# Kernel optimization log

Measured on AMD Instinct MI355X. Metric: run time of the kernel, lower is better.

## Reference

```python
import jax, jax.numpy as jnp
import numpy as np


def setup_inputs() -> dict:
    key = jax.random.key(0)
    k1, k2, k3 = jax.random.split(key, 3)
    B, S, H = 64, 2048, 1024
    return {
        "dec_state_h": jax.random.normal(k1, (B, H), dtype=jnp.float32),
        "dec_state_c": jax.random.normal(k2, (B, H), dtype=jnp.float32),
        "enc_output": jax.random.normal(k3, (B, S, H), dtype=jnp.float32),
    }


def reference(dec_state_h, dec_state_c, enc_output):
    # dec_state: [B, H] = h + c  (Luong-style combined decoder state)
    dec_state = dec_state_h + dec_state_c
    # score[b, s] = sum_h enc_output[b, s, h] * dec_state[b, h]  -> [B, S, 1]
    score = jnp.einsum("bsh,bh->bs", enc_output, dec_state)[..., None]
    # softmax over the sequence axis
    attention_weights = jax.nn.softmax(score, axis=1)  # [B, S, 1]
    # context[b, h] = sum_s attn[b, s] * enc_output[b, s, h]
    context_vector = jnp.einsum("bs,bsh->bh", attention_weights[..., 0], enc_output)
    return context_vector, attention_weights
```

## Files before the change

### kernel.cpp

```cpp
#include <hip/hip_runtime.h>
#include <math.h>

#define B 64
#define S 2048
#define H 1024
#define SPLIT 16
#define ROWS_PER_BLOCK (S / SPLIT)
#define THREADS 256
#define WAVES 4
#define ROWS_PER_WAVE (ROWS_PER_BLOCK / WAVES)

__global__ __launch_bounds__(THREADS)
void luong_pass1(const float* __restrict__ dec_h,
                 const float* __restrict__ dec_c,
                 const float* __restrict__ enc,
                 float* __restrict__ attn_raw,
                 float* __restrict__ ctx_part,
                 float* __restrict__ mz_part) {
  const int bid  = blockIdx.x;
  const int b    = bid / SPLIT;
  const int sp   = bid % SPLIT;
  const int t    = threadIdx.x;
  const int w    = t >> 6;
  const int lane = t & 63;

  float4 dec[4];
  const float4* dh = (const float4*)(dec_h + (size_t)b * H);
  const float4* dc = (const float4*)(dec_c + (size_t)b * H);
#pragma unroll
  for (int c = 0; c < 4; ++c) {
    float4 a  = dh[c * 64 + lane];
    float4 bb = dc[c * 64 + lane];
    dec[c] = make_float4(a.x + bb.x, a.y + bb.y, a.z + bb.z, a.w + bb.w);
  }

  float m = -INFINITY;
  float Z = 0.f;
  float ctx[16];
#pragma unroll
  for (int k = 0; k < 16; ++k) ctx[k] = 0.f;

  const int s_base = sp * ROWS_PER_BLOCK + w;
  for (int r = 0; r < ROWS_PER_WAVE; ++r) {
    const int s = s_base + r * WAVES;
    const float4* erow = (const float4*)(enc + ((size_t)b * S + s) * H);
    float4 e[4];
#pragma unroll
    for (int c = 0; c < 4; ++c) e[c] = erow[c * 64 + lane];

    float partial = 0.f;
#pragma unroll
    for (int c = 0; c < 4; ++c)
      partial += e[c].x * dec[c].x + e[c].y * dec[c].y +
                 e[c].z * dec[c].z + e[c].w * dec[c].w;
#pragma unroll
    for (int off = 32; off >= 1; off >>= 1)
      partial += __shfl_xor(partial, off, 64);
    const float score = partial;

    if (lane == 0) attn_raw[b * S + s] = score;

    if (score > m) {
      const float f = expf(m - score);
      Z *= f;
#pragma unroll
      for (int k = 0; k < 16; ++k) ctx[k] *= f;
      m = score;
    }
    const float p = expf(score - m);
    Z += p;
#pragma unroll
    for (int c = 0; c < 4; ++c) {
      ctx[c * 4 + 0] += p * e[c].x;
      ctx[c * 4 + 1] += p * e[c].y;
      ctx[c * 4 + 2] += p * e[c].z;
      ctx[c * 4 + 3] += p * e[c].w;
    }
  }

  __shared__ float ctx_lds[WAVES][H];
  __shared__ float mzs[WAVES][2];
#pragma unroll
  for (int c = 0; c < 4; ++c) {
    float4 v = make_float4(ctx[c * 4 + 0], ctx[c * 4 + 1],
                           ctx[c * 4 + 2], ctx[c * 4 + 3]);
    ((float4*)&ctx_lds[w][c * 256])[lane] = v;
  }
  if (lane == 0) { mzs[w][0] = m; mzs[w][1] = Z; }
  __syncthreads();

  const float M = fmaxf(fmaxf(mzs[0][0], mzs[1][0]),
                        fmaxf(mzs[2][0], mzs[3][0]));
  float fac[WAVES];
  float Zb = 0.f;
#pragma unroll
  for (int i = 0; i < WAVES; ++i) {
    fac[i] = expf(mzs[i][0] - M);
    Zb += mzs[i][1] * fac[i];
  }

  float* outp = ctx_part + ((size_t)b * SPLIT + sp) * H;
#pragma unroll
  for (int q = 0; q < 4; ++q) {
    const int h = q * 256 + t;
    float v = 0.f;
#pragma unroll
    for (int i = 0; i < WAVES; ++i) v += ctx_lds[i][h] * fac[i];
    outp[h] = v;
  }
  if (t == 0) {
    mz_part[(b * SPLIT + sp) * 2 + 0] = M;
    mz_part[(b * SPLIT + sp) * 2 + 1] = Zb;
  }
}

__global__ __launch_bounds__(256)
void luong_combine(const float* __restrict__ ctx_part,
                   const float* __restrict__ mz_part,
                   float* __restrict__ ctx_out,
                   float* __restrict__ mz_final) {
  const int b = blockIdx.x;
  const int t = threadIdx.x;

  float m_i[SPLIT], z_i[SPLIT];
  float M = -INFINITY;
#pragma unroll
  for (int i = 0; i < SPLIT; ++i) {
    m_i[i] = mz_part[(b * SPLIT + i) * 2 + 0];
    z_i[i] = mz_part[(b * SPLIT + i) * 2 + 1];
    M = fmaxf(M, m_i[i]);
  }
  float fac[SPLIT];
  float Z = 0.f;
#pragma unroll
  for (int i = 0; i < SPLIT; ++i) {
    fac[i] = expf(m_i[i] - M);
    Z += z_i[i] * fac[i];
  }
  const float invZ = 1.f / Z;

#pragma unroll
  for (int q = 0; q < 4; ++q) {
    const int h = q * 256 + t;
    float v = 0.f;
#pragma unroll
    for (int i = 0; i < SPLIT; ++i)
      v += ctx_part[((size_t)(b * SPLIT + i)) * H + h] * fac[i];
    ctx_out[(size_t)b * H + h] = v * invZ;
  }
  if (t == 0) {
    mz_final[2 * b + 0] = M;
    mz_final[2 * b + 1] = Z;
  }
}

__global__ __launch_bounds__(256)
void luong_fixup(float* __restrict__ attn,
                 const float* __restrict__ mz_final) {
  const int idx = blockIdx.x * blockDim.x + threadIdx.x;
  if (idx >= B * S) return;
  const int b = idx >> 11;
  const float M = mz_final[2 * b + 0];
  const float Z = mz_final[2 * b + 1];
  attn[idx] = expf(attn[idx] - M) / Z;
}

extern "C" void kernel_launch(void* const* d_in, const int* in_sizes, int n_in,
                              void* d_out, int out_size, void* d_ws, size_t ws_size,
                              hipStream_t stream) {
  const float* dec_h = (const float*)d_in[0];
  const float* dec_c = (const float*)d_in[1];
  const float* enc   = (const float*)d_in[2];

  float* ctx_out = (float*)d_out;
  float* attn    = (float*)d_out + B * H;

  float* ctx_part = (float*)d_ws;
  float* mz_part  = ctx_part + (size_t)B * SPLIT * H;
  float* mz_final = mz_part + (size_t)B * SPLIT * 2;

  luong_pass1<<<B * SPLIT, THREADS, 0, stream>>>(dec_h, dec_c, enc, attn,
                                                 ctx_part, mz_part);
  luong_combine<<<B, 256, 0, stream>>>(ctx_part, mz_part, ctx_out, mz_final);
  luong_fixup<<<(B * S + 255) / 256, 256, 0, stream>>>(attn, mz_final);
}
```

Baseline: 114.6 us.

## Software-pipeline encoder row loads in pairs with double buffering in pass1

The main loop now handles two sequence rows per step and double-buffers register loads, fetching the next pair while the current one is reduced. Interleaving the two shuffle reductions and sharing one max/rescale per pair cuts the serial dependency chain and exposes more memory-level parallelism. Launch bounds now request 4 blocks per CU. The extra buffers raise register use, which could hurt occupancy or cause spills.

```diff
diff --git a/kernel.cpp b/kernel.cpp
--- a/kernel.cpp
+++ b/kernel.cpp
@@ -9,8 +9,60 @@
 #define THREADS 256
 #define WAVES 4
 #define ROWS_PER_WAVE (ROWS_PER_BLOCK / WAVES)
-
-__global__ __launch_bounds__(THREADS)
+#define PAIRS (ROWS_PER_WAVE / 2)
+
+
+#define LOADP(EBUF, pidx) do {                                                  \
+    const int sL0_ = s_base + ((pidx) * 2)     * WAVES;                         \
+    const int sL1_ = s_base + ((pidx) * 2 + 1) * WAVES;                         \
+    const float4* r0_ = (const float4*)(enc + ((size_t)b * S + sL0_) * H);      \
+    const float4* r1_ = (const float4*)(enc + ((size_t)b * S + sL1_) * H);      \
+    _Pragma("unroll")                                                           \
+    for (int c_ = 0; c_ < 4; ++c_) {                                            \
+      EBUF[c_]     = r0_[c_ * 64 + lane];                                       \
+      EBUF[4 + c_] = r1_[c_ * 64 + lane];                                       \
+    }                                                                           \
+  } while (0)
+
+#define PROC(EBUF, pidx) do {                                                   \
+    float p0_ = 0.f, p1_ = 0.f;                                                 \
+    _Pragma("unroll")                                                           \
+    for (int c_ = 0; c_ < 4; ++c_) {                                            \
+      p0_ += EBUF[c_].x * dec[c_].x + EBUF[c_].y * dec[c_].y +                  \
+             EBUF[c_].z * dec[c_].z + EBUF[c_].w * dec[c_].w;                   \
+      p1_ += EBUF[4+c_].x * dec[c_].x + EBUF[4+c_].y * dec[c_].y +              \
+             EBUF[4+c_].z * dec[c_].z + EBUF[4+c_].w * dec[c_].w;               \
+    }                                                                           \
+    _Pragma("unroll")                                                           \
+    for (int off_ = 32; off_ >= 1; off_ >>= 1) {                                \
+      p0_ += __shfl_xor(p0_, off_, 64);                                         \
+      p1_ += __shfl_xor(p1_, off_, 64);                                         \
+    }                                                                           \
+    const int sA_ = s_base + ((pidx) * 2) * WAVES;                              \
+    if (lane == 0) {                                                            \
+      attn_raw[b * S + sA_]         = p0_;                                      \
+      attn_raw[b * S + sA_ + WAVES] = p1_;                                      \
+    }                                                                           \
+    const float mn_ = fmaxf(m, fmaxf(p0_, p1_));                                \
+    if (mn_ > m) {                                                              \
+      const float f_ = expf(m - mn_);                                           \
+      Z *= f_;                                                                  \
+      _Pragma("unroll")                                                         \
+      for (int k_ = 0; k_ < 16; ++k_) ctx[k_] *= f_;                            \
+      m = mn_;                                                                  \
+    }                                                                           \
+    const float e0_ = expf(p0_ - m), e1_ = expf(p1_ - m);                       \
+    Z += e0_ + e1_;                                                             \
+    _Pragma("unroll")                                                           \
+    for (int c_ = 0; c_ < 4; ++c_) {                                            \
+      ctx[c_*4+0] += e0_ * EBUF[c_].x + e1_ * EBUF[4+c_].x;                     \
+      ctx[c_*4+1] += e0_ * EBUF[c_].y + e1_ * EBUF[4+c_].y;                     \
+      ctx[c_*4+2] += e0_ * EBUF[c_].z + e1_ * EBUF[4+c_].z;                     \
+      ctx[c_*4+3] += e0_ * EBUF[c_].w + e1_ * EBUF[4+c_].w;                     \
+    }                                                                           \
+  } while (0)
+
+__global__ __launch_bounds__(THREADS, 4)
 void luong_pass1(const float* __restrict__ dec_h,
                  const float* __restrict__ dec_c,
                  const float* __restrict__ enc,
@@ -41,41 +93,14 @@
   for (int k = 0; k < 16; ++k) ctx[k] = 0.f;
 
   const int s_base = sp * ROWS_PER_BLOCK + w;
-  for (int r = 0; r < ROWS_PER_WAVE; ++r) {
-    const int s = s_base + r * WAVES;
-    const float4* erow = (const float4*)(enc + ((size_t)b * S + s) * H);
-    float4 e[4];
-#pragma unroll
-    for (int c = 0; c < 4; ++c) e[c] = erow[c * 64 + lane];
-
-    float partial = 0.f;
-#pragma unroll
-    for (int c = 0; c < 4; ++c)
-      partial += e[c].x * dec[c].x + e[c].y * dec[c].y +
-                 e[c].z * dec[c].z + e[c].w * dec[c].w;
-#pragma unroll
-    for (int off = 32; off >= 1; off >>= 1)
-      partial += __shfl_xor(partial, off, 64);
-    const float score = partial;
-
-    if (lane == 0) attn_raw[b * S + s] = score;
-
-    if (score > m) {
-      const float f = expf(m - score);
-      Z *= f;
-#pragma unroll
-      for (int k = 0; k < 16; ++k) ctx[k] *= f;
-      m = score;
-    }
-    const float p = expf(score - m);
-    Z += p;
-#pragma unroll
-    for (int c = 0; c < 4; ++c) {
-      ctx[c * 4 + 0] += p * e[c].x;
-      ctx[c * 4 + 1] += p * e[c].y;
-      ctx[c * 4 + 2] += p * e[c].z;
-      ctx[c * 4 + 3] += p * e[c].w;
-    }
+
+  float4 eA[8], eB[8];
+  LOADP(eA, 0);
+  for (int p2 = 0; p2 < PAIRS / 2; ++p2) {
+    LOADP(eB, 2 * p2 + 1);
+    PROC(eA, 2 * p2);
+    if (p2 < PAIRS / 2 - 1) LOADP(eA, 2 * p2 + 2);
+    PROC(eB, 2 * p2 + 1);
   }
 
   __shared__ float ctx_lds[WAVES][H];
```

After: 175.0 us. +52.7%, slower.

## Software-pipeline encoder row loads with triple register buffering in pass1

Applied to the files above, without the earlier changes.

Restructures the per-wave row loop so each row's float4 loads are issued two rows ahead, into a rotating set of three register buffers, while the current row's dot product, online softmax and context accumulation run. It also adds a minimum-occupancy hint to the launch bounds. The goal is to hide global memory latency in this bandwidth-bound streaming kernel. The cost is higher register pressure from the extra buffers, which the occupancy hint might force into spills.

```diff
diff --git a/kernel.cpp b/kernel.cpp
--- a/kernel.cpp
+++ b/kernel.cpp
@@ -10,7 +10,7 @@
 #define WAVES 4
 #define ROWS_PER_WAVE (ROWS_PER_BLOCK / WAVES)
 
-__global__ __launch_bounds__(THREADS)
+__global__ __launch_bounds__(THREADS, 4)
 void luong_pass1(const float* __restrict__ dec_h,
                  const float* __restrict__ dec_c,
                  const float* __restrict__ enc,
@@ -41,42 +41,59 @@
   for (int k = 0; k < 16; ++k) ctx[k] = 0.f;
 
   const int s_base = sp * ROWS_PER_BLOCK + w;
-  for (int r = 0; r < ROWS_PER_WAVE; ++r) {
-    const int s = s_base + r * WAVES;
-    const float4* erow = (const float4*)(enc + ((size_t)b * S + s) * H);
-    float4 e[4];
-#pragma unroll
-    for (int c = 0; c < 4; ++c) e[c] = erow[c * 64 + lane];
-
-    float partial = 0.f;
-#pragma unroll
-    for (int c = 0; c < 4; ++c)
-      partial += e[c].x * dec[c].x + e[c].y * dec[c].y +
-                 e[c].z * dec[c].z + e[c].w * dec[c].w;
-#pragma unroll
-    for (int off = 32; off >= 1; off >>= 1)
-      partial += __shfl_xor(partial, off, 64);
-    const float score = partial;
-
-    if (lane == 0) attn_raw[b * S + s] = score;
-
-    if (score > m) {
-      const float f = expf(m - score);
-      Z *= f;
-#pragma unroll
-      for (int k = 0; k < 16; ++k) ctx[k] *= f;
-      m = score;
-    }
-    const float p = expf(score - m);
-    Z += p;
-#pragma unroll
-    for (int c = 0; c < 4; ++c) {
-      ctx[c * 4 + 0] += p * e[c].x;
-      ctx[c * 4 + 1] += p * e[c].y;
-      ctx[c * 4 + 2] += p * e[c].z;
-      ctx[c * 4 + 3] += p * e[c].w;
-    }
-  }
+  const float4* ebase = (const float4*)(enc + ((size_t)b * S + s_base) * H);
+
+  float4 buf[3][4];
+
+#define LOADR(SL, R) do {                                                      \
+    const float4* rp_ = ebase + (size_t)(R) * (WAVES * (H / 4));               \
+    _Pragma("unroll")                                                          \
+    for (int c_ = 0; c_ < 4; ++c_) buf[SL][c_] = rp_[c_ * 64 + lane];          \
+  } while (0)
+
+#define PROCR(SL, R) do {                                                      \
+    float p_ = 0.f;                                                            \
+    _Pragma("unroll")                                                          \
+    for (int c_ = 0; c_ < 4; ++c_)                                             \
+      p_ += buf[SL][c_].x * dec[c_].x + buf[SL][c_].y * dec[c_].y +            \
+            buf[SL][c_].z * dec[c_].z + buf[SL][c_].w * dec[c_].w;             \
+    _Pragma("unroll")                                                          \
+    for (int off_ = 32; off_ >= 1; off_ >>= 1)                                 \
+      p_ += __shfl_xor(p_, off_, 64);                                          \
+    if (lane == 0) attn_raw[b * S + s_base + (R) * WAVES] = p_;                \
+    if (p_ > m) {                                                              \
+      const float f_ = expf(m - p_);                                           \
+      Z *= f_;                                                                 \
+      _Pragma("unroll")                                                        \
+      for (int k_ = 0; k_ < 16; ++k_) ctx[k_] *= f_;                           \
+      m = p_;                                                                  \
+    }                                                                          \
+    const float e_ = expf(p_ - m);                                             \
+    Z += e_;                                                                   \
+    _Pragma("unroll")                                                          \
+    for (int c_ = 0; c_ < 4; ++c_) {                                           \
+      ctx[c_ * 4 + 0] += e_ * buf[SL][c_].x;                                   \
+      ctx[c_ * 4 + 1] += e_ * buf[SL][c_].y;                                   \
+      ctx[c_ * 4 + 2] += e_ * buf[SL][c_].z;                                   \
+      ctx[c_ * 4 + 3] += e_ * buf[SL][c_].w;                                   \
+    }                                                                          \
+  } while (0)
+
+  LOADR(0, 0);
+  LOADR(1, 1);
+  for (int i = 0; i < ROWS_PER_WAVE - 2; i += 3) {
+    LOADR(2, i + 2);
+    PROCR(0, i);
+    LOADR(0, i + 3);
+    PROCR(1, i + 1);
+    LOADR(1, i + 4);
+    PROCR(2, i + 2);
+  }
+  PROCR(0, ROWS_PER_WAVE - 2);
+  PROCR(1, ROWS_PER_WAVE - 1);
+
+#undef LOADR
+#undef PROCR
 
   __shared__ float ctx_lds[WAVES][H];
   __shared__ float mzs[WAVES][2];
```

New measurement: 116.1 us. Within noise of the previous version (+1.4%).

## Fuse combine and fixup into pass1 via last-block atomic counter

Applied to the files above, without the earlier changes.

The three launches (partial attention, per-batch combine, softmax fixup) become one kernel. Each block bumps a per-batch atomic counter after writing its partials, and the last block of each batch merges the split results and normalises the attention row. This removes two kernel launches and their gaps, and the reduction now runs as soon as a batch's partials are ready. In exchange it adds a memset launch, threadfences and an atomic per block, and the tail work is serialised onto 64 last blocks.

```diff
diff --git a/kernel.cpp b/kernel.cpp
--- a/kernel.cpp
+++ b/kernel.cpp
@@ -5,18 +5,20 @@
 #define S 2048
 #define H 1024
 #define SPLIT 16
-#define ROWS_PER_BLOCK (S / SPLIT)
+#define RPB (S / SPLIT)
 #define THREADS 256
 #define WAVES 4
-#define ROWS_PER_WAVE (ROWS_PER_BLOCK / WAVES)
+#define RPW (RPB / WAVES)
 
 __global__ __launch_bounds__(THREADS)
-void luong_pass1(const float* __restrict__ dec_h,
+void luong_fused(const float* __restrict__ dec_h,
                  const float* __restrict__ dec_c,
                  const float* __restrict__ enc,
-                 float* __restrict__ attn_raw,
+                 float* __restrict__ ctx_out,
+                 float* __restrict__ attn,
                  float* __restrict__ ctx_part,
-                 float* __restrict__ mz_part) {
+                 float* __restrict__ mz_part,
+                 unsigned* __restrict__ cnt) {
   const int bid  = blockIdx.x;
   const int b    = bid / SPLIT;
   const int sp   = bid % SPLIT;
@@ -25,13 +27,15 @@
   const int lane = t & 63;
 
   float4 dec[4];
-  const float4* dh = (const float4*)(dec_h + (size_t)b * H);
-  const float4* dc = (const float4*)(dec_c + (size_t)b * H);
+  {
+    const float4* dh = (const float4*)(dec_h + (size_t)b * H);
+    const float4* dc = (const float4*)(dec_c + (size_t)b * H);
 #pragma unroll
-  for (int c = 0; c < 4; ++c) {
-    float4 a  = dh[c * 64 + lane];
-    float4 bb = dc[c * 64 + lane];
-    dec[c] = make_float4(a.x + bb.x, a.y + bb.y, a.z + bb.z, a.w + bb.w);
+    for (int c = 0; c < 4; ++c) {
+      float4 a  = dh[c * 64 + lane];
+      float4 bb = dc[c * 64 + lane];
+      dec[c] = make_float4(a.x + bb.x, a.y + bb.y, a.z + bb.z, a.w + bb.w);
+    }
   }
 
   float m = -INFINITY;
@@ -40,41 +44,41 @@
 #pragma unroll
   for (int k = 0; k < 16; ++k) ctx[k] = 0.f;
 
-  const int s_base = sp * ROWS_PER_BLOCK + w;
-  for (int r = 0; r < ROWS_PER_WAVE; ++r) {
-    const int s = s_base + r * WAVES;
-    const float4* erow = (const float4*)(enc + ((size_t)b * S + s) * H);
+  const int s_base = sp * RPB + w;
+  const float4* ebase = (const float4*)(enc + ((size_t)b * S + s_base) * H);
+
+  for (int r = 0; r < RPW; ++r) {
+    const float4* rp = ebase + (size_t)r * (WAVES * (H / 4));
     float4 e[4];
 #pragma unroll
-    for (int c = 0; c < 4; ++c) e[c] = erow[c * 64 + lane];
+    for (int c = 0; c < 4; ++c) e[c] = rp[c * 64 + lane];
 
-    float partial = 0.f;
+    float p = 0.f;
 #pragma unroll
     for (int c = 0; c < 4; ++c)
-      partial += e[c].x * dec[c].x + e[c].y * dec[c].y +
-                 e[c].z * dec[c].z + e[c].w * dec[c].w;
+      p += e[c].x * dec[c].x + e[c].y * dec[c].y +
+           e[c].z * dec[c].z + e[c].w * dec[c].w;
 #pragma unroll
     for (int off = 32; off >= 1; off >>= 1)
-      partial += __shfl_xor(partial, off, 64);
-    const float score = partial;
+      p += __shfl_xor(p, off, 64);
 
-    if (lane == 0) attn_raw[b * S + s] = score;
+    if (lane == 0) attn[b * S + s_base + r * WAVES] = p;
 
-    if (score > m) {
-      const float f = expf(m - score);
+    if (p > m) {
+      const float f = expf(m - p);
       Z *= f;
 #pragma unroll
       for (int k = 0; k < 16; ++k) ctx[k] *= f;
-      m = score;
+      m = p;
     }
-    const float p = expf(score - m);
-    Z += p;
+    const float e_ = expf(p - m);
+    Z += e_;
 #pragma unroll
     for (int c = 0; c < 4; ++c) {
-      ctx[c * 4 + 0] += p * e[c].x;
-      ctx[c * 4 + 1] += p * e[c].y;
-      ctx[c * 4 + 2] += p * e[c].z;
-      ctx[c * 4 + 3] += p * e[c].w;
+      ctx[c * 4 + 0] += e_ * e[c].x;
+      ctx[c * 4 + 1] += e_ * e[c].y;
+      ctx[c * 4 + 2] += e_ * e[c].z;
+      ctx[c * 4 + 3] += e_ * e[c].w;
     }
   }
 
@@ -89,55 +93,55 @@
   if (lane == 0) { mzs[w][0] = m; mzs[w][1] = Z; }
   __syncthreads();
 
-  const float M = fmaxf(fmaxf(mzs[0][0], mzs[1][0]),
-                        fmaxf(mzs[2][0], mzs[3][0]));
-  float fac[WAVES];
-  float Zb = 0.f;
+  {
+    const float Mb = fmaxf(fmaxf(mzs[0][0], mzs[1][0]),
+                           fmaxf(mzs[2][0], mzs[3][0]));
+    float fac[WAVES];
+    float Zb = 0.f;
 #pragma unroll
-  for (int i = 0; i < WAVES; ++i) {
-    fac[i] = expf(mzs[i][0] - M);
-    Zb += mzs[i][1] * fac[i];
+    for (int i = 0; i < WAVES; ++i) {
+      fac[i] = expf(mzs[i][0] - Mb);
+      Zb += mzs[i][1] * fac[i];
+    }
+    float* outp = ctx_part + ((size_t)b * SPLIT + sp) * H;
+#pragma unroll
+    for (int q = 0; q < 4; ++q) {
+      const int h = q * 256 + t;
+      float v = 0.f;
+#pragma unroll
+      for (int i = 0; i < WAVES; ++i) v += ctx_lds[i][h] * fac[i];
+      outp[h] = v;
+    }
+    if (t == 0) {
+      mz_part[(b * SPLIT + sp) * 2 + 0] = Mb;
+      mz_part[(b * SPLIT + sp) * 2 + 1] = Zb;
+    }
   }
 
-  float* outp = ctx_part + ((size_t)b * SPLIT + sp) * H;
-#pragma unroll
-  for (int q = 0; q < 4; ++q) {
-    const int h = q * 256 + t;
-    float v = 0.f;
-#pragma unroll
-    for (int i = 0; i < WAVES; ++i) v += ctx_lds[i][h] * fac[i];
-    outp[h] = v;
+  __threadfence();
+  __shared__ unsigned last;
+  if (t == 0) {
+    unsigned old = __hip_atomic_fetch_add(&cnt[b], 1u,
+                                          __ATOMIC_ACQ_REL,
+                                          __HIP_MEMORY_SCOPE_AGENT);
+    last = (old == SPLIT - 1) ? 1u : 0u;
   }
-  if (t == 0) {
-    mz_part[(b * SPLIT + sp) * 2 + 0] = M;
-    mz_part[(b * SPLIT + sp) * 2 + 1] = Zb;
-  }
-}
+  __syncthreads();
+  if (!last) return;
+  __threadfence();
 
-__global__ __launch_bounds__(256)
-void luong_combine(const float* __restrict__ ctx_part,
-                   const float* __restrict__ mz_part,
-                   float* __restrict__ ctx_out,
-                   float* __restrict__ mz_final) {
-  const int b = blockIdx.x;
-  const int t = threadIdx.x;
-
-  float m_i[SPLIT], z_i[SPLIT];
+  const float* mzb = mz_part + (size_t)b * SPLIT * 2;
   float M = -INFINITY;
 #pragma unroll
-  for (int i = 0; i < SPLIT; ++i) {
-    m_i[i] = mz_part[(b * SPLIT + i) * 2 + 0];
-    z_i[i] = mz_part[(b * SPLIT + i) * 2 + 1];
-    M = fmaxf(M, m_i[i]);
-  }
+  for (int i = 0; i < SPLIT; ++i) M = fmaxf(M, mzb[2 * i]);
   float fac[SPLIT];
-  float Z = 0.f;
+  float Zt = 0.f;
 #pragma unroll
   for (int i = 0; i < SPLIT; ++i) {
-    fac[i] = expf(m_i[i] - M);
-    Z += z_i[i] * fac[i];
+    fac[i] = expf(mzb[2 * i] - M);
+    Zt += mzb[2 * i + 1] * fac[i];
   }
-  const float invZ = 1.f / Z;
+  const float invZ = 1.f / Zt;
 
 #pragma unroll
   for (int q = 0; q < 4; ++q) {
@@ -145,24 +149,15 @@
     float v = 0.f;
 #pragma unroll
     for (int i = 0; i < SPLIT; ++i)
-      v += ctx_part[((size_t)(b * SPLIT + i)) * H + h] * fac[i];
+      v += ctx_part[((size_t)b * SPLIT + i) * H + h] * fac[i];
     ctx_out[(size_t)b * H + h] = v * invZ;
   }
-  if (t == 0) {
-    mz_final[2 * b + 0] = M;
-    mz_final[2 * b + 1] = Z;
+
+#pragma unroll
+  for (int k = 0; k < 8; ++k) {
+    const size_t idx = (size_t)b * S + k * 256 + t;
+    attn[idx] = expf(attn[idx] - M) * invZ;
   }
-}
-
-__global__ __launch_bounds__(256)
-void luong_fixup(float* __restrict__ attn,
-                 const float* __restrict__ mz_final) {
-  const int idx = blockIdx.x * blockDim.x + threadIdx.x;
-  if (idx >= B * S) return;
-  const int b = idx >> 11;
-  const float M = mz_final[2 * b + 0];
-  const float Z = mz_final[2 * b + 1];
-  attn[idx] = expf(attn[idx] - M) / Z;
 }
 
 extern "C" void kernel_launch(void* const* d_in, const int* in_sizes, int n_in,
@@ -175,12 +170,12 @@
   float* ctx_out = (float*)d_out;
   float* attn    = (float*)d_out + B * H;
 
-  float* ctx_part = (float*)d_ws;
-  float* mz_part  = ctx_part + (size_t)B * SPLIT * H;
-  float* mz_final = mz_part + (size_t)B * SPLIT * 2;
+  float*    ctx_part = (float*)d_ws;
+  float*    mz_part  = ctx_part + (size_t)B * SPLIT * H;
+  unsigned* cnt      = (unsigned*)(mz_part + (size_t)B * SPLIT * 2);
 
-  luong_pass1<<<B * SPLIT, THREADS, 0, stream>>>(dec_h, dec_c, enc, attn,
-                                                 ctx_part, mz_part);
-  luong_combine<<<B, 256, 0, stream>>>(ctx_part, mz_part, ctx_out, mz_final);
-  luong_fixup<<<(B * S + 255) / 256, 256, 0, stream>>>(attn, mz_final);
+  hipMemsetAsync(cnt, 0, B * sizeof(unsigned), stream);
+  luong_fused<<<B * SPLIT, THREADS, 0, stream>>>(dec_h, dec_c, enc,
+                                                 ctx_out, attn,
+                                                 ctx_part, mz_part, cnt);
 }
```

After: 320.1 us. +179.3%, slower.
